# Performance work log

Measured on AMD Instinct MI355X. Metric: run time of the kernel, lower is better.

The kernel has to match this reference:

```python
import jax, jax.numpy as jnp
import numpy as np

NBINS = 256  # skimage threshold_otsu default
RGB_W = jnp.array([0.2989, 0.5870, 0.1140], dtype=jnp.float32)  # tf.image.rgb_to_grayscale weights


def threshold_otsu(img):
    """Global Otsu threshold over all pixels, matching skimage.filters.threshold_otsu."""
    vmin = img.min()
    vmax = img.max()
    edges = jnp.linspace(vmin, vmax, NBINS + 1)
    centers = (edges[:-1] + edges[1:]) * 0.5
    hist = jnp.histogram(img.ravel(), bins=edges)[0].astype(jnp.float32)
    # class probabilities / cumulative weights
    w1 = jnp.cumsum(hist)                      # weight of class <= t
    w2 = jnp.cumsum(hist[::-1])[::-1]          # weight of class > t
    hc = hist * centers
    s1 = jnp.cumsum(hc)
    s2 = jnp.cumsum(hc[::-1])[::-1]
    m1 = s1 / jnp.maximum(w1, 1.0)
    m2 = s2 / jnp.maximum(w2, 1.0)
    # inter-class variance at each split point
    var12 = w1[:-1] * w2[1:] * (m1[:-1] - m2[1:]) ** 2
    idx = jnp.argmax(var12)
    return centers[idx]


def setup_inputs() -> dict:
    key = jax.random.key(0)
    inputs = jax.random.uniform(key, (32, 128, 2048, 3), dtype=jnp.float32)
    return {"inputs": inputs}


def reference(inputs) -> jnp.ndarray:
    # rgb_to_grayscale on first 3 channels, keep channel dim -> [B,H,W,1]
    gray = jnp.einsum('bhwc,c->bhw', inputs[..., :3].astype(jnp.float32), RGB_W)[..., None]
    thresh = threshold_otsu(gray)
    binarized = (gray > thresh).astype(jnp.float32)   # [B,H,W,1]
    # channels == 3 -> tile grayscale binarization back to 3 channels
    binarized = jnp.tile(binarized, (1, 1, 1, 3))
    return binarized
```

## Files before the change

### kernel.cpp

```cpp
#include <hip/hip_runtime.h>

static constexpr int HIST_OFF   = 2;
static constexpr int EDGES_OFF  = 258;
static constexpr int VMIN_OFF   = 515;
static constexpr int DELTA_OFF  = 516;
static constexpr int INVD_OFF   = 517;
static constexpr int THRESH_OFF = 518;
static constexpr size_t GRAY_BYTE_OFF = 4096;

typedef float nfloat4 __attribute__((ext_vector_type(4)));

__device__ __forceinline__ unsigned fkey(float x) {
    unsigned u = __float_as_uint(x);
    return (u & 0x80000000u) ? ~u : (u | 0x80000000u);
}
__device__ __forceinline__ float keyf(unsigned k) {
    return (k & 0x80000000u) ? __uint_as_float(k & 0x7FFFFFFFu)
                             : __uint_as_float(~k);
}

__device__ __forceinline__ float gray1(float r, float g, float b) {
    float t0 = __fmul_rn(r, 0.2989f);
    float t1 = __fmul_rn(g, 0.5870f);
    float t2 = __fmul_rn(b, 0.1140f);
    return __fadd_rn(__fadd_rn(t0, t1), t2);
}

__device__ __forceinline__ float permf(int dst_addr, float v) {
    return __int_as_float(
        __builtin_amdgcn_ds_permute(dst_addr, __float_as_int(v)));
}
__device__ __forceinline__ float selk(float a, float b, float c, int k) {
    return (k == 0) ? a : ((k == 1) ? b : c);
}

__global__ void init_kernel(unsigned* __restrict__ wsu) {
    int i = threadIdx.x;
    if (i < 256) wsu[HIST_OFF + i] = 0u;
    if (i == 0) { wsu[0] = 0xFFFFFFFFu; wsu[1] = 0u; }
}

__global__ void __launch_bounds__(256)
gray_minmax_fast(const float* __restrict__ in, float* __restrict__ gray,
                 unsigned* __restrict__ wsu, int npix4) {
    __shared__ unsigned smn[4], smx[4];
    const nfloat4* in4 = (const nfloat4*)in;
    nfloat4* gray4 = (nfloat4*)gray;
    const int nf4 = npix4 * 3;
    const int lane = threadIdx.x & 63;
    const int gw = (blockIdx.x * blockDim.x + threadIdx.x) >> 6;
    unsigned mn = 0xFFFFFFFFu, mx = 0u;

    const int s3 = lane % 3;
    const int ka = (3 - s3) % 3;
    const int kb = (ka + 1) % 3;
    const int kc = (ka + 2) % 3;
    const int da = 4 * ((64 * ka + lane) / 3);
    const int db = 4 * ((64 * kb + lane) / 3);
    const int dc = 4 * ((64 * kc + lane) / 3);

    const int wbase4 = gw * 768;

    nfloat4 c[4][3];
    bool full[4];
#pragma unroll
    for (int r = 0; r < 4; ++r) {
        int rb = wbase4 + r * 192;
        full[r] = (rb + 192 <= nf4);
        if (full[r]) {
#pragma unroll
            for (int k = 0; k < 3; ++k)
                c[r][k] = __builtin_nontemporal_load(&in4[rb + 64 * k + lane]);
        }
    }
#pragma unroll
    for (int r = 0; r < 4; ++r) {
        const int gbase = gw * 256 + r * 64;
        nfloat4 d0, d1, d2;
        bool have = false;
        if (full[r]) {
            d0.x = permf(da, selk(c[r][0].x, c[r][1].x, c[r][2].x, ka));
            d0.y = permf(da, selk(c[r][0].y, c[r][1].y, c[r][2].y, ka));
            d0.z = permf(da, selk(c[r][0].z, c[r][1].z, c[r][2].z, ka));
            d0.w = permf(da, selk(c[r][0].w, c[r][1].w, c[r][2].w, ka));
            d1.x = permf(db, selk(c[r][0].x, c[r][1].x, c[r][2].x, kb));
            d1.y = permf(db, selk(c[r][0].y, c[r][1].y, c[r][2].y, kb));
            d1.z = permf(db, selk(c[r][0].z, c[r][1].z, c[r][2].z, kb));
            d1.w = permf(db, selk(c[r][0].w, c[r][1].w, c[r][2].w, kb));
            d2.x = permf(dc, selk(c[r][0].x, c[r][1].x, c[r][2].x, kc));
            d2.y = permf(dc, selk(c[r][0].y, c[r][1].y, c[r][2].y, kc));
            d2.z = permf(dc, selk(c[r][0].z, c[r][1].z, c[r][2].z, kc));
            d2.w = permf(dc, selk(c[r][0].w, c[r][1].w, c[r][2].w, kc));
            have = true;
        } else {
            int g = gbase + lane;
            if (g < npix4) {
                const nfloat4* p = in4 + (size_t)g * 3;
                d0 = p[0]; d1 = p[1]; d2 = p[2];
                have = true;
            }
        }
        if (have) {
            float g0 = gray1(d0.x, d0.y, d0.z);
            float g1 = gray1(d0.w, d1.x, d1.y);
            float g2 = gray1(d1.z, d1.w, d2.x);
            float g3 = gray1(d2.y, d2.z, d2.w);
            gray4[gbase + lane] = (nfloat4){g0, g1, g2, g3};
            unsigned k0 = fkey(g0), k1 = fkey(g1), k2 = fkey(g2), k3 = fkey(g3);
            mn = min(mn, min(min(k0, k1), min(k2, k3)));
            mx = max(mx, max(max(k0, k1), max(k2, k3)));
        }
    }
    for (int off = 32; off > 0; off >>= 1) {
        mn = min(mn, (unsigned)__shfl_xor((int)mn, off, 64));
        mx = max(mx, (unsigned)__shfl_xor((int)mx, off, 64));
    }
    int wave = threadIdx.x >> 6;
    if ((threadIdx.x & 63) == 0) { smn[wave] = mn; smx[wave] = mx; }
    __syncthreads();
    if (threadIdx.x == 0) {
        mn = min(min(smn[0], smn[1]), min(smn[2], smn[3]));
        mx = max(max(smx[0], smx[1]), max(smx[2], smx[3]));
        atomicMin(&wsu[0], mn);
        atomicMax(&wsu[1], mx);
    }
}

__global__ void __launch_bounds__(256)
gray_minmax_generic(const float* __restrict__ in, float* __restrict__ gray,
                    unsigned* __restrict__ wsu, int npix4) {
    __shared__ unsigned smn[4], smx[4];
    const float4* in4 = (const float4*)in;
    const int stride = gridDim.x * blockDim.x;
    unsigned mn = 0xFFFFFFFFu, mx = 0u;
    for (int t = blockIdx.x * blockDim.x + threadIdx.x; t < npix4; t += stride) {
        const float4* p = in4 + (size_t)t * 3;
        float4 c0 = p[0], c1 = p[1], c2 = p[2];
        float g0 = gray1(c0.x, c0.y, c0.z);
        float g1 = gray1(c0.w, c1.x, c1.y);
        float g2 = gray1(c1.z, c1.w, c2.x);
        float g3 = gray1(c2.y, c2.z, c2.w);
        if (gray) ((float4*)gray)[t] = make_float4(g0, g1, g2, g3);
        unsigned k0 = fkey(g0), k1 = fkey(g1), k2 = fkey(g2), k3 = fkey(g3);
        mn = min(mn, min(min(k0, k1), min(k2, k3)));
        mx = max(mx, max(max(k0, k1), max(k2, k3)));
    }
    for (int off = 32; off > 0; off >>= 1) {
        mn = min(mn, (unsigned)__shfl_xor((int)mn, off, 64));
        mx = max(mx, (unsigned)__shfl_xor((int)mx, off, 64));
    }
    int wave = threadIdx.x >> 6;
    if ((threadIdx.x & 63) == 0) { smn[wave] = mn; smx[wave] = mx; }
    __syncthreads();
    if (threadIdx.x == 0) {
        mn = min(min(smn[0], smn[1]), min(smn[2], smn[3]));
        mx = max(max(smx[0], smx[1]), max(smx[2], smx[3]));
        atomicMin(&wsu[0], mn);
        atomicMax(&wsu[1], mx);
    }
}

__global__ void edges_kernel(const unsigned* __restrict__ wsu,
                             float* __restrict__ wsf) {
    float vmin = keyf(wsu[0]);
    float vmax = keyf(wsu[1]);
    float delta = __fdiv_rn(__fsub_rn(vmax, vmin), 256.0f);
    int i = threadIdx.x;
    if (i <= 256) {
        float e = (i == 256) ? vmax
                             : __fadd_rn(vmin, __fmul_rn((float)i, delta));
        wsf[EDGES_OFF + i] = e;
    }
    if (i == 0) {
        wsf[VMIN_OFF]  = vmin;
        wsf[DELTA_OFF] = delta;
        wsf[INVD_OFF]  = (delta > 0.0f) ? __fdiv_rn(1.0f, delta) : 0.0f;
    }
}

__device__ __forceinline__ void bin4(float x0, float x1, float x2, float x3,
                                     const float* eds, float vmin, float invd,
                                     unsigned* lh) {
    float xs[4] = {x0, x1, x2, x3};
#pragma unroll
    for (int j = 0; j < 4; ++j) {
        float x = xs[j];
        int b = (int)(__fmul_rn(__fsub_rn(x, vmin), invd));
        b = b < 0 ? 0 : (b > 255 ? 255 : b);
        while (b < 255 && x >= eds[b + 1]) ++b;
        while (b > 0 && x < eds[b]) --b;
        atomicAdd(&lh[b], 1u);
    }
}

__global__ void __launch_bounds__(256)
hist_kernel(const float* __restrict__ gray, const float* __restrict__ in,
            const float* __restrict__ wsf, unsigned* __restrict__ wsu,
            int npix4) {
    __shared__ float eds[257];
    __shared__ unsigned lh[256];
    for (int i = threadIdx.x; i < 257; i += blockDim.x)
        eds[i] = wsf[EDGES_OFF + i];
    if (threadIdx.x < 256) lh[threadIdx.x] = 0u;
    __syncthreads();
    const float vmin = eds[0];
    const float invd = wsf[INVD_OFF];
    const int stride = gridDim.x * blockDim.x;
    const int base = blockIdx.x * blockDim.x + threadIdx.x;

    if (gray && base + 7 * stride < npix4) {
        float4 g[8];
#pragma unroll
        for (int j = 0; j < 8; ++j) g[j] = ((const float4*)gray)[base + j * stride];
#pragma unroll
        for (int j = 0; j < 8; ++j)
            bin4(g[j].x, g[j].y, g[j].z, g[j].w, eds, vmin, invd, lh);
    } else {
        for (int t = base; t < npix4; t += stride) {
            float4 g4;
            if (gray) g4 = ((const float4*)gray)[t];
            else {
                const float4* p = (const float4*)in + (size_t)t * 3;
                float4 c0 = p[0], c1 = p[1], c2 = p[2];
                g4 = make_float4(gray1(c0.x, c0.y, c0.z),
                                 gray1(c0.w, c1.x, c1.y),
                                 gray1(c1.z, c1.w, c2.x),
                                 gray1(c2.y, c2.z, c2.w));
            }
            bin4(g4.x, g4.y, g4.z, g4.w, eds, vmin, invd, lh);
        }
    }
    __syncthreads();
    if (threadIdx.x < 256 && lh[threadIdx.x] != 0u)
        atomicAdd(&wsu[HIST_OFF + threadIdx.x], lh[threadIdx.x]);
}

__global__ void otsu_kernel(const unsigned* __restrict__ wsu,
                            float* __restrict__ wsf) {
    __shared__ float histf[256];
    __shared__ float centers[256];
    __shared__ float w2a[256];
    __shared__ float s2a[256];
    int i = threadIdx.x;
    float e0 = wsf[EDGES_OFF + i];
    float e1 = wsf[EDGES_OFF + i + 1];
    centers[i] = __fmul_rn(__fadd_rn(e0, e1), 0.5f);
    histf[i] = (float)wsu[HIST_OFF + i];
    __syncthreads();
    if (i == 0) {
        float w = 0.0f, s = 0.0f;
        for (int t = 255; t >= 0; --t) {
            w = __fadd_rn(w, histf[t]);
            s = __fadd_rn(s, __fmul_rn(histf[t], centers[t]));
            w2a[t] = w;
            s2a[t] = s;
        }
        float w1 = 0.0f, s1 = 0.0f, best = -1.0f;
        int bidx = 0;
        for (int t = 0; t < 255; ++t) {
            w1 = __fadd_rn(w1, histf[t]);
            s1 = __fadd_rn(s1, __fmul_rn(histf[t], centers[t]));
            float m1 = __fdiv_rn(s1, fmaxf(w1, 1.0f));
            float m2 = __fdiv_rn(s2a[t + 1], fmaxf(w2a[t + 1], 1.0f));
            float d  = __fsub_rn(m1, m2);
            float v  = __fmul_rn(__fmul_rn(w1, w2a[t + 1]), __fmul_rn(d, d));
            if (v > best) { best = v; bidx = t; }
        }
        wsf[THRESH_OFF] = centers[bidx];
    }
}

__global__ void __launch_bounds__(256)
binarize_fast(const float* __restrict__ gray, const float* __restrict__ wsf,
              float* __restrict__ out, int npix4) {
    const float thr = wsf[THRESH_OFF];
    const nfloat4* gray4 = (const nfloat4*)gray;
    nfloat4* out4 = (nfloat4*)out;
    const int lane = threadIdx.x & 63;
    const int gw = (blockIdx.x * blockDim.x + threadIdx.x) >> 6;

    const int ma = lane / 3,         qa = lane % 3;
    const int mb = (64 + lane) / 3,  qb = (64 + lane) % 3;
    const int mc = (128 + lane) / 3, qc = (128 + lane) % 3;

    nfloat4 g[4];
    bool full[4];
#pragma unroll
    for (int r = 0; r < 4; ++r) {
        int gbase = gw * 256 + r * 64;
        full[r] = (gbase + 64 <= npix4);
        if (full[r]) g[r] = gray4[gbase + lane];
    }
#pragma unroll
    for (int r = 0; r < 4; ++r) {
        const int gbase = gw * 256 + r * 64;
        if (full[r]) {
            unsigned u = (g[r].x > thr ? 1u : 0u) |
                         (g[r].y > thr ? 0x100u : 0u) |
                         (g[r].z > thr ? 0x10000u : 0u) |
                         (g[r].w > thr ? 0x1000000u : 0u);
            const int rb = 3 * gbase;
#pragma unroll
            for (int k = 0; k < 3; ++k) {
                int m = (k == 0) ? ma : (k == 1) ? mb : mc;
                int q = (k == 0) ? qa : (k == 1) ? qb : qc;
                unsigned w = (unsigned)__builtin_amdgcn_ds_bpermute(4 * m,
                                                                    (int)u);
                float h0 = (w & 0xffu)        ? 1.0f : 0.0f;
                float h1 = (w & 0xff00u)      ? 1.0f : 0.0f;
                float h2 = (w & 0xff0000u)    ? 1.0f : 0.0f;
                float h3 = (w & 0xff000000u)  ? 1.0f : 0.0f;
                nfloat4 o;
                o.x = (q == 0) ? h0 : (q == 1) ? h1 : h2;
                o.y = (q == 0) ? h0 : (q == 1) ? h1 : h3;
                o.z = (q == 0) ? h0 : (q == 1) ? h2 : h3;
                o.w = (q == 0) ? h1 : (q == 1) ? h2 : h3;
                __builtin_nontemporal_store(o, &out4[rb + 64 * k + lane]);
            }
        } else {
            int t = gbase + lane;
            if (t < npix4) {
                nfloat4 gg = gray4[t];
                float b0 = (gg.x > thr) ? 1.0f : 0.0f;
                float b1 = (gg.y > thr) ? 1.0f : 0.0f;
                float b2 = (gg.z > thr) ? 1.0f : 0.0f;
                float b3 = (gg.w > thr) ? 1.0f : 0.0f;
                nfloat4* o = out4 + (size_t)t * 3;
                __builtin_nontemporal_store((nfloat4){b0, b0, b0, b1}, &o[0]);
                __builtin_nontemporal_store((nfloat4){b1, b1, b2, b2}, &o[1]);
                __builtin_nontemporal_store((nfloat4){b2, b3, b3, b3}, &o[2]);
            }
        }
    }
}

__global__ void __launch_bounds__(256)
binarize_generic(const float* __restrict__ gray, const float* __restrict__ in,
                 const float* __restrict__ wsf, float* __restrict__ out,
                 int npix4) {
    const float thr = wsf[THRESH_OFF];
    const int stride = gridDim.x * blockDim.x;
    nfloat4* out4 = (nfloat4*)out;
    for (int t = blockIdx.x * blockDim.x + threadIdx.x; t < npix4; t += stride) {
        float4 g4;
        if (gray) g4 = ((const float4*)gray)[t];
        else {
            const float4* p = (const float4*)in + (size_t)t * 3;
            float4 c0 = p[0], c1 = p[1], c2 = p[2];
            g4 = make_float4(gray1(c0.x, c0.y, c0.z),
                             gray1(c0.w, c1.x, c1.y),
                             gray1(c1.z, c1.w, c2.x),
                             gray1(c2.y, c2.z, c2.w));
        }
        float b0 = (g4.x > thr) ? 1.0f : 0.0f;
        float b1 = (g4.y > thr) ? 1.0f : 0.0f;
        float b2 = (g4.z > thr) ? 1.0f : 0.0f;
        float b3 = (g4.w > thr) ? 1.0f : 0.0f;
        nfloat4* o = out4 + (size_t)t * 3;
        o[0] = (nfloat4){b0, b0, b0, b1};
        o[1] = (nfloat4){b1, b1, b2, b2};
        o[2] = (nfloat4){b2, b3, b3, b3};
    }
}

extern "C" void kernel_launch(void* const* d_in, const int* in_sizes, int n_in,
                              void* d_out, int out_size, void* d_ws,
                              size_t ws_size, hipStream_t stream) {
    const float* in = (const float*)d_in[0];
    float* out = (float*)d_out;
    int npix  = out_size / 3;
    int npix4 = npix / 4;
    unsigned* wsu = (unsigned*)d_ws;
    float* wsf = (float*)d_ws;
    size_t need = GRAY_BYTE_OFF + (size_t)npix * sizeof(float);
    float* gray = (ws_size >= need)
                      ? (float*)((char*)d_ws + GRAY_BYTE_OFF)
                      : nullptr;

    hipLaunchKernelGGL(init_kernel, dim3(1), dim3(256), 0, stream, wsu);
    int fblocks = (npix4 + 1023) / 1024;
    if (gray) {
        hipLaunchKernelGGL(gray_minmax_fast, dim3(fblocks), dim3(256), 0,
                           stream, in, gray, wsu, npix4);
    } else {
        hipLaunchKernelGGL(gray_minmax_generic, dim3(2048), dim3(256), 0,
                           stream, in, gray, wsu, npix4);
    }
    hipLaunchKernelGGL(edges_kernel, dim3(1), dim3(320), 0, stream, wsu, wsf);
    hipLaunchKernelGGL(hist_kernel, dim3(1024), dim3(256), 0, stream,
                       gray, in, wsf, wsu, npix4);
    hipLaunchKernelGGL(otsu_kernel, dim3(1), dim3(256), 0, stream, wsu, wsf);
    if (gray) {
        hipLaunchKernelGGL(binarize_fast, dim3(fblocks), dim3(256), 0, stream,
                           gray, wsf, out, npix4);
    } else {
        hipLaunchKernelGGL(binarize_generic, dim3(2048), dim3(256), 0, stream,
                           gray, in, wsf, out, npix4);
    }
}
```

Baseline: 287.2 us.

## Fuse gray/minmax, histogram, Otsu and binarize into one cooperative persistent kernel

Replaces the multi-kernel pipeline with a single cooperative kernel. Each wave holds its grayscale values in registers across two grid-wide syncs, so the gray buffer is never written to or re-read from global memory. The Otsu threshold is computed redundantly per block. The input loads are software-pipelined with double buffering. The cost is two grid syncs, a fixed 1024-block grid whose tiles must cover all pixels, and a redundant serial Otsu scan in every block.

```diff
diff --git a/kernel.cpp b/kernel.cpp
--- a/kernel.cpp
+++ b/kernel.cpp
@@ -1,4 +1,7 @@
 #include <hip/hip_runtime.h>
+#include <hip/hip_cooperative_groups.h>
+
+namespace cg = cooperative_groups;
 
 static constexpr int HIST_OFF   = 2;
 static constexpr int EDGES_OFF  = 258;
@@ -18,20 +21,21 @@
     return (k & 0x80000000u) ? __uint_as_float(k & 0x7FFFFFFFu)
                              : __uint_as_float(~k);
 }
-
 __device__ __forceinline__ float gray1(float r, float g, float b) {
     float t0 = __fmul_rn(r, 0.2989f);
     float t1 = __fmul_rn(g, 0.5870f);
     float t2 = __fmul_rn(b, 0.1140f);
     return __fadd_rn(__fadd_rn(t0, t1), t2);
 }
-
 __device__ __forceinline__ float permf(int dst_addr, float v) {
     return __int_as_float(
         __builtin_amdgcn_ds_permute(dst_addr, __float_as_int(v)));
 }
 __device__ __forceinline__ float selk(float a, float b, float c, int k) {
     return (k == 0) ? a : ((k == 1) ? b : c);
+}
+__device__ __forceinline__ unsigned aload(const unsigned* p) {
+    return __hip_atomic_load(p, __ATOMIC_RELAXED, __HIP_MEMORY_SCOPE_AGENT);
 }
 
 __global__ void init_kernel(unsigned* __restrict__ wsu) {
@@ -40,57 +44,67 @@
     if (i == 0) { wsu[0] = 0xFFFFFFFFu; wsu[1] = 0u; }
 }
 
-__global__ void __launch_bounds__(256)
-gray_minmax_fast(const float* __restrict__ in, float* __restrict__ gray,
-                 unsigned* __restrict__ wsu, int npix4) {
-    __shared__ unsigned smn[4], smx[4];
+__global__ void __launch_bounds__(256, 4)
+fused_kernel(const float* __restrict__ in, float* __restrict__ out,
+             unsigned* __restrict__ wsu, int npix4) {
+    cg::grid_group grid = cg::this_grid();
+    __shared__ float eds[257];
+    __shared__ unsigned lh[256];
+    __shared__ float histf[256], centers[256], w2a[256], s2a[256];
+    __shared__ unsigned smn[4], smx[4], skey[2];
+    __shared__ float sthr;
+
     const nfloat4* in4 = (const nfloat4*)in;
-    nfloat4* gray4 = (nfloat4*)gray;
-    const int nf4 = npix4 * 3;
+    nfloat4* out4 = (nfloat4*)out;
     const int lane = threadIdx.x & 63;
     const int gw = (blockIdx.x * blockDim.x + threadIdx.x) >> 6;
-    unsigned mn = 0xFFFFFFFFu, mx = 0u;
+    const int gtile = gw * 512;
+    const int wbase4 = gw * 1536;
 
     const int s3 = lane % 3;
-    const int ka = (3 - s3) % 3;
-    const int kb = (ka + 1) % 3;
-    const int kc = (ka + 2) % 3;
+    const int ka = (3 - s3) % 3, kb = (ka + 1) % 3, kc = (ka + 2) % 3;
     const int da = 4 * ((64 * ka + lane) / 3);
     const int db = 4 * ((64 * kb + lane) / 3);
     const int dc = 4 * ((64 * kc + lane) / 3);
-
-    const int wbase4 = gw * 768;
-
-    nfloat4 c[4][3];
-    bool full[4];
-#pragma unroll
-    for (int r = 0; r < 4; ++r) {
-        int rb = wbase4 + r * 192;
-        full[r] = (rb + 192 <= nf4);
-        if (full[r]) {
+    const int ma = lane / 3,         qa = lane % 3;
+    const int mb = (64 + lane) / 3,  qb = (64 + lane) % 3;
+    const int mc = (128 + lane) / 3, qc = (128 + lane) % 3;
+
+    bool full[8];
+#pragma unroll
+    for (int r = 0; r < 8; ++r) full[r] = (gtile + r * 64 + 64 <= npix4);
+
+    float gr[8][4];
+    unsigned mn = 0xFFFFFFFFu, mx = 0u;
+    nfloat4 cb[2][3];
+    if (full[0]) {
+#pragma unroll
+        for (int k = 0; k < 3; ++k) cb[0][k] = in4[wbase4 + 64 * k + lane];
+    }
+#pragma unroll
+    for (int r = 0; r < 8; ++r) {
+        const int cur = r & 1, nxt = cur ^ 1;
+        if (r + 1 < 8 && full[r + 1]) {
 #pragma unroll
             for (int k = 0; k < 3; ++k)
-                c[r][k] = __builtin_nontemporal_load(&in4[rb + 64 * k + lane]);
-        }
-    }
-#pragma unroll
-    for (int r = 0; r < 4; ++r) {
-        const int gbase = gw * 256 + r * 64;
+                cb[nxt][k] = in4[wbase4 + (r + 1) * 192 + 64 * k + lane];
+        }
+        const int gbase = gtile + r * 64;
         nfloat4 d0, d1, d2;
         bool have = false;
         if (full[r]) {
-            d0.x = permf(da, selk(c[r][0].x, c[r][1].x, c[r][2].x, ka));
-            d0.y = permf(da, selk(c[r][0].y, c[r][1].y, c[r][2].y, ka));
-            d0.z = permf(da, selk(c[r][0].z, c[r][1].z, c[r][2].z, ka));
-            d0.w = permf(da, selk(c[r][0].w, c[r][1].w, c[r][2].w, ka));
-            d1.x = permf(db, selk(c[r][0].x, c[r][1].x, c[r][2].x, kb));
-            d1.y = permf(db, selk(c[r][0].y, c[r][1].y, c[r][2].y, kb));
-            d1.z = permf(db, selk(c[r][0].z, c[r][1].z, c[r][2].z, kb));
-            d1.w = permf(db, selk(c[r][0].w, c[r][1].w, c[r][2].w, kb));
-            d2.x = permf(dc, selk(c[r][0].x, c[r][1].x, c[r][2].x, kc));
-            d2.y = permf(dc, selk(c[r][0].y, c[r][1].y, c[r][2].y, kc));
-            d2.z = permf(dc, selk(c[r][0].z, c[r][1].z, c[r][2].z, kc));
-            d2.w = permf(dc, selk(c[r][0].w, c[r][1].w, c[r][2].w, kc));
+            d0.x = permf(da, selk(cb[cur][0].x, cb[cur][1].x, cb[cur][2].x, ka));
+            d0.y = permf(da, selk(cb[cur][0].y, cb[cur][1].y, cb[cur][2].y, ka));
+            d0.z = permf(da, selk(cb[cur][0].z, cb[cur][1].z, cb[cur][2].z, ka));
+            d0.w = permf(da, selk(cb[cur][0].w, cb[cur][1].w, cb[cur][2].w, ka));
+            d1.x = permf(db, selk(cb[cur][0].x, cb[cur][1].x, cb[cur][2].x, kb));
+            d1.y = permf(db, selk(cb[cur][0].y, cb[cur][1].y, cb[cur][2].y, kb));
+            d1.z = permf(db, selk(cb[cur][0].z, cb[cur][1].z, cb[cur][2].z, kb));
+            d1.w = permf(db, selk(cb[cur][0].w, cb[cur][1].w, cb[cur][2].w, kb));
+            d2.x = permf(dc, selk(cb[cur][0].x, cb[cur][1].x, cb[cur][2].x, kc));
+            d2.y = permf(dc, selk(cb[cur][0].y, cb[cur][1].y, cb[cur][2].y, kc));
+            d2.z = permf(dc, selk(cb[cur][0].z, cb[cur][1].z, cb[cur][2].z, kc));
+            d2.w = permf(dc, selk(cb[cur][0].w, cb[cur][1].w, cb[cur][2].w, kc));
             have = true;
         } else {
             int g = gbase + lane;
@@ -101,28 +115,137 @@
             }
         }
         if (have) {
-            float g0 = gray1(d0.x, d0.y, d0.z);
-            float g1 = gray1(d0.w, d1.x, d1.y);
-            float g2 = gray1(d1.z, d1.w, d2.x);
-            float g3 = gray1(d2.y, d2.z, d2.w);
-            gray4[gbase + lane] = (nfloat4){g0, g1, g2, g3};
-            unsigned k0 = fkey(g0), k1 = fkey(g1), k2 = fkey(g2), k3 = fkey(g3);
+            gr[r][0] = gray1(d0.x, d0.y, d0.z);
+            gr[r][1] = gray1(d0.w, d1.x, d1.y);
+            gr[r][2] = gray1(d1.z, d1.w, d2.x);
+            gr[r][3] = gray1(d2.y, d2.z, d2.w);
+            unsigned k0 = fkey(gr[r][0]), k1 = fkey(gr[r][1]);
+            unsigned k2 = fkey(gr[r][2]), k3 = fkey(gr[r][3]);
             mn = min(mn, min(min(k0, k1), min(k2, k3)));
             mx = max(mx, max(max(k0, k1), max(k2, k3)));
+        } else {
+            gr[r][0] = gr[r][1] = gr[r][2] = gr[r][3] = 0.0f;
         }
     }
     for (int off = 32; off > 0; off >>= 1) {
         mn = min(mn, (unsigned)__shfl_xor((int)mn, off, 64));
         mx = max(mx, (unsigned)__shfl_xor((int)mx, off, 64));
     }
-    int wave = threadIdx.x >> 6;
-    if ((threadIdx.x & 63) == 0) { smn[wave] = mn; smx[wave] = mx; }
+    {
+        int wave = threadIdx.x >> 6;
+        if ((threadIdx.x & 63) == 0) { smn[wave] = mn; smx[wave] = mx; }
+        __syncthreads();
+        if (threadIdx.x == 0) {
+            unsigned bmn = min(min(smn[0], smn[1]), min(smn[2], smn[3]));
+            unsigned bmx = max(max(smx[0], smx[1]), max(smx[2], smx[3]));
+            atomicMin(&wsu[0], bmn);
+            atomicMax(&wsu[1], bmx);
+        }
+    }
+    grid.sync();
+
+    if (threadIdx.x == 0) { skey[0] = aload(&wsu[0]); skey[1] = aload(&wsu[1]); }
+    __syncthreads();
+    const float vmin = keyf(skey[0]);
+    const float vmax = keyf(skey[1]);
+    const float delta = __fdiv_rn(__fsub_rn(vmax, vmin), 256.0f);
+    const float invd = (delta > 0.0f) ? __fdiv_rn(1.0f, delta) : 0.0f;
+    if (threadIdx.x < 256)
+        eds[threadIdx.x] =
+            __fadd_rn(vmin, __fmul_rn((float)threadIdx.x, delta));
+    if (threadIdx.x == 0) eds[256] = vmax;
+    if (threadIdx.x < 256) lh[threadIdx.x] = 0u;
+    __syncthreads();
+
+#pragma unroll
+    for (int r = 0; r < 8; ++r) {
+        const int g = gtile + r * 64 + lane;
+        if (full[r] || g < npix4) {
+#pragma unroll
+            for (int j = 0; j < 4; ++j) {
+                float x = gr[r][j];
+                int b = (int)(__fmul_rn(__fsub_rn(x, vmin), invd));
+                b = b < 0 ? 0 : (b > 255 ? 255 : b);
+                while (b < 255 && x >= eds[b + 1]) ++b;
+                while (b > 0 && x < eds[b]) --b;
+                atomicAdd(&lh[b], 1u);
+            }
+        }
+    }
+    __syncthreads();
+    if (threadIdx.x < 256 && lh[threadIdx.x] != 0u)
+        atomicAdd(&wsu[HIST_OFF + threadIdx.x], lh[threadIdx.x]);
+    grid.sync();
+
+    if (threadIdx.x < 256) {
+        float e0 = eds[threadIdx.x], e1 = eds[threadIdx.x + 1];
+        centers[threadIdx.x] = __fmul_rn(__fadd_rn(e0, e1), 0.5f);
+        histf[threadIdx.x] = (float)aload(&wsu[HIST_OFF + threadIdx.x]);
+    }
     __syncthreads();
     if (threadIdx.x == 0) {
-        mn = min(min(smn[0], smn[1]), min(smn[2], smn[3]));
-        mx = max(max(smx[0], smx[1]), max(smx[2], smx[3]));
-        atomicMin(&wsu[0], mn);
-        atomicMax(&wsu[1], mx);
+        float w = 0.0f, s = 0.0f;
+        for (int t = 255; t >= 0; --t) {
+            w = __fadd_rn(w, histf[t]);
+            s = __fadd_rn(s, __fmul_rn(histf[t], centers[t]));
+            w2a[t] = w;
+            s2a[t] = s;
+        }
+        float w1 = 0.0f, s1 = 0.0f, best = -1.0f;
+        int bidx = 0;
+        for (int t = 0; t < 255; ++t) {
+            w1 = __fadd_rn(w1, histf[t]);
+            s1 = __fadd_rn(s1, __fmul_rn(histf[t], centers[t]));
+            float m1 = __fdiv_rn(s1, fmaxf(w1, 1.0f));
+            float m2 = __fdiv_rn(s2a[t + 1], fmaxf(w2a[t + 1], 1.0f));
+            float d  = __fsub_rn(m1, m2);
+            float v  = __fmul_rn(__fmul_rn(w1, w2a[t + 1]), __fmul_rn(d, d));
+            if (v > best) { best = v; bidx = t; }
+        }
+        sthr = centers[bidx];
+    }
+    __syncthreads();
+    const float thr = sthr;
+
+#pragma unroll
+    for (int r = 0; r < 8; ++r) {
+        const int gbase = gtile + r * 64;
+        if (full[r]) {
+            unsigned u = (gr[r][0] > thr ? 1u : 0u) |
+                         (gr[r][1] > thr ? 0x100u : 0u) |
+                         (gr[r][2] > thr ? 0x10000u : 0u) |
+                         (gr[r][3] > thr ? 0x1000000u : 0u);
+            const int rb = 3 * gbase;
+#pragma unroll
+            for (int k = 0; k < 3; ++k) {
+                int m = (k == 0) ? ma : (k == 1) ? mb : mc;
+                int q = (k == 0) ? qa : (k == 1) ? qb : qc;
+                unsigned w = (unsigned)__builtin_amdgcn_ds_bpermute(4 * m,
+                                                                    (int)u);
+                float h0 = (w & 0xffu)       ? 1.0f : 0.0f;
+                float h1 = (w & 0xff00u)     ? 1.0f : 0.0f;
+                float h2 = (w & 0xff0000u)   ? 1.0f : 0.0f;
+                float h3 = (w & 0xff000000u) ? 1.0f : 0.0f;
+                nfloat4 o;
+                o.x = (q == 0) ? h0 : (q == 1) ? h1 : h2;
+                o.y = (q == 0) ? h0 : (q == 1) ? h1 : h3;
+                o.z = (q == 0) ? h0 : (q == 1) ? h2 : h3;
+                o.w = (q == 0) ? h1 : (q == 1) ? h2 : h3;
+                __builtin_nontemporal_store(o, &out4[rb + 64 * k + lane]);
+            }
+        } else {
+            int t = gbase + lane;
+            if (t < npix4) {
+                float b0 = (gr[r][0] > thr) ? 1.0f : 0.0f;
+                float b1 = (gr[r][1] > thr) ? 1.0f : 0.0f;
+                float b2 = (gr[r][2] > thr) ? 1.0f : 0.0f;
+                float b3 = (gr[r][3] > thr) ? 1.0f : 0.0f;
+                nfloat4* o = out4 + (size_t)t * 3;
+                __builtin_nontemporal_store((nfloat4){b0, b0, b0, b1}, &o[0]);
+                __builtin_nontemporal_store((nfloat4){b1, b1, b2, b2}, &o[1]);
+                __builtin_nontemporal_store((nfloat4){b2, b3, b3, b3}, &o[2]);
+            }
+        }
     }
 }
 
@@ -206,29 +329,16 @@
     const float vmin = eds[0];
     const float invd = wsf[INVD_OFF];
     const int stride = gridDim.x * blockDim.x;
-    const int base = blockIdx.x * blockDim.x + threadIdx.x;
-
-    if (gray && base + 7 * stride < npix4) {
-        float4 g[8];
-#pragma unroll
-        for (int j = 0; j < 8; ++j) g[j] = ((const float4*)gray)[base + j * stride];
-#pragma unroll
-        for (int j = 0; j < 8; ++j)
-            bin4(g[j].x, g[j].y, g[j].z, g[j].w, eds, vmin, invd, lh);
-    } else {
-        for (int t = base; t < npix4; t += stride) {
-            float4 g4;
-            if (gray) g4 = ((const float4*)gray)[t];
-            else {
-                const float4* p = (const float4*)in + (size_t)t * 3;
-                float4 c0 = p[0], c1 = p[1], c2 = p[2];
-                g4 = make_float4(gray1(c0.x, c0.y, c0.z),
-                                 gray1(c0.w, c1.x, c1.y),
-                                 gray1(c1.z, c1.w, c2.x),
-                                 gray1(c2.y, c2.z, c2.w));
-            }
-            bin4(g4.x, g4.y, g4.z, g4.w, eds, vmin, invd, lh);
-        }
+    for (int t = blockIdx.x * blockDim.x + threadIdx.x; t < npix4; t += stride) {
+        float4 g4;
+        if (gray) g4 = ((const float4*)gray)[t];
+        else {
+            const float4* p = (const float4*)in + (size_t)t * 3;
+            float4 c0 = p[0], c1 = p[1], c2 = p[2];
+            g4 = make_float4(gray1(c0.x, c0.y, c0.z), gray1(c0.w, c1.x, c1.y),
+                             gray1(c1.z, c1.w, c2.x), gray1(c2.y, c2.z, c2.w));
+        }
+        bin4(g4.x, g4.y, g4.z, g4.w, eds, vmin, invd, lh);
     }
     __syncthreads();
     if (threadIdx.x < 256 && lh[threadIdx.x] != 0u)
@@ -267,70 +377,6 @@
             if (v > best) { best = v; bidx = t; }
         }
         wsf[THRESH_OFF] = centers[bidx];
-    }
-}
-
-__global__ void __launch_bounds__(256)
-binarize_fast(const float* __restrict__ gray, const float* __restrict__ wsf,
-              float* __restrict__ out, int npix4) {
-    const float thr = wsf[THRESH_OFF];
-    const nfloat4* gray4 = (const nfloat4*)gray;
-    nfloat4* out4 = (nfloat4*)out;
-    const int lane = threadIdx.x & 63;
-    const int gw = (blockIdx.x * blockDim.x + threadIdx.x) >> 6;
-
-    const int ma = lane / 3,         qa = lane % 3;
-    const int mb = (64 + lane) / 3,  qb = (64 + lane) % 3;
-    const int mc = (128 + lane) / 3, qc = (128 + lane) % 3;
-
-    nfloat4 g[4];
-    bool full[4];
-#pragma unroll
-    for (int r = 0; r < 4; ++r) {
-        int gbase = gw * 256 + r * 64;
-        full[r] = (gbase + 64 <= npix4);
-        if (full[r]) g[r] = gray4[gbase + lane];
-    }
-#pragma unroll
-    for (int r = 0; r < 4; ++r) {
-        const int gbase = gw * 256 + r * 64;
-        if (full[r]) {
-            unsigned u = (g[r].x > thr ? 1u : 0u) |
-                         (g[r].y > thr ? 0x100u : 0u) |
-                         (g[r].z > thr ? 0x10000u : 0u) |
-                         (g[r].w > thr ? 0x1000000u : 0u);
-            const int rb = 3 * gbase;
-#pragma unroll
-            for (int k = 0; k < 3; ++k) {
-                int m = (k == 0) ? ma : (k == 1) ? mb : mc;
-                int q = (k == 0) ? qa : (k == 1) ? qb : qc;
-                unsigned w = (unsigned)__builtin_amdgcn_ds_bpermute(4 * m,
-                                                                    (int)u);
-                float h0 = (w & 0xffu)        ? 1.0f : 0.0f;
-                float h1 = (w & 0xff00u)      ? 1.0f : 0.0f;
-                float h2 = (w & 0xff0000u)    ? 1.0f : 0.0f;
-                float h3 = (w & 0xff000000u)  ? 1.0f : 0.0f;
-                nfloat4 o;
-                o.x = (q == 0) ? h0 : (q == 1) ? h1 : h2;
-                o.y = (q == 0) ? h0 : (q == 1) ? h1 : h3;
-                o.z = (q == 0) ? h0 : (q == 1) ? h2 : h3;
-                o.w = (q == 0) ? h1 : (q == 1) ? h2 : h3;
-                __builtin_nontemporal_store(o, &out4[rb + 64 * k + lane]);
-            }
-        } else {
-            int t = gbase + lane;
-            if (t < npix4) {
-                nfloat4 gg = gray4[t];
-                float b0 = (gg.x > thr) ? 1.0f : 0.0f;
-                float b1 = (gg.y > thr) ? 1.0f : 0.0f;
-                float b2 = (gg.z > thr) ? 1.0f : 0.0f;
-                float b3 = (gg.w > thr) ? 1.0f : 0.0f;
-                nfloat4* o = out4 + (size_t)t * 3;
-                __builtin_nontemporal_store((nfloat4){b0, b0, b0, b1}, &o[0]);
-                __builtin_nontemporal_store((nfloat4){b1, b1, b2, b2}, &o[1]);
-                __builtin_nontemporal_store((nfloat4){b2, b3, b3, b3}, &o[2]);
-            }
-        }
     }
 }
 
@@ -347,10 +393,8 @@
         else {
             const float4* p = (const float4*)in + (size_t)t * 3;
             float4 c0 = p[0], c1 = p[1], c2 = p[2];
-            g4 = make_float4(gray1(c0.x, c0.y, c0.z),
-                             gray1(c0.w, c1.x, c1.y),
-                             gray1(c1.z, c1.w, c2.x),
-                             gray1(c2.y, c2.z, c2.w));
+            g4 = make_float4(gray1(c0.x, c0.y, c0.z), gray1(c0.w, c1.x, c1.y),
+                             gray1(c1.z, c1.w, c2.x), gray1(c2.y, c2.z, c2.w));
         }
         float b0 = (g4.x > thr) ? 1.0f : 0.0f;
         float b1 = (g4.y > thr) ? 1.0f : 0.0f;
@@ -372,29 +416,24 @@
     int npix4 = npix / 4;
     unsigned* wsu = (unsigned*)d_ws;
     float* wsf = (float*)d_ws;
+
+    hipLaunchKernelGGL(init_kernel, dim3(1), dim3(256), 0, stream, wsu);
+
+    void* args[] = {(void*)&in, (void*)&out, (void*)&wsu, (void*)&npix4};
+    hipError_t err = hipLaunchCooperativeKernel(
+        (const void*)fused_kernel, dim3(1024), dim3(256), args, 0, stream);
+    if (err == hipSuccess) return;
+
     size_t need = GRAY_BYTE_OFF + (size_t)npix * sizeof(float);
     float* gray = (ws_size >= need)
                       ? (float*)((char*)d_ws + GRAY_BYTE_OFF)
                       : nullptr;
-
-    hipLaunchKernelGGL(init_kernel, dim3(1), dim3(256), 0, stream, wsu);
-    int fblocks = (npix4 + 1023) / 1024;
-    if (gray) {
-        hipLaunchKernelGGL(gray_minmax_fast, dim3(fblocks), dim3(256), 0,
-                           stream, in, gray, wsu, npix4);
-    } else {
-        hipLaunchKernelGGL(gray_minmax_generic, dim3(2048), dim3(256), 0,
-                           stream, in, gray, wsu, npix4);
-    }
+    hipLaunchKernelGGL(gray_minmax_generic, dim3(2048), dim3(256), 0, stream,
+                       in, gray, wsu, npix4);
     hipLaunchKernelGGL(edges_kernel, dim3(1), dim3(320), 0, stream, wsu, wsf);
     hipLaunchKernelGGL(hist_kernel, dim3(1024), dim3(256), 0, stream,
                        gray, in, wsf, wsu, npix4);
     hipLaunchKernelGGL(otsu_kernel, dim3(1), dim3(256), 0, stream, wsu, wsf);
-    if (gray) {
-        hipLaunchKernelGGL(binarize_fast, dim3(fblocks), dim3(256), 0, stream,
-                           gray, wsf, out, npix4);
-    } else {
-        hipLaunchKernelGGL(binarize_generic, dim3(2048), dim3(256), 0, stream,
-                           gray, in, wsf, out, npix4);
-    }
-}
+    hipLaunchKernelGGL(binarize_generic, dim3(2048), dim3(256), 0, stream,
+                       gray, in, wsf, out, npix4);
+}
```

New measurement: 457.0 us. 59.1% more time.

## Stage gray/minmax input through LDS with async global-to-LDS double-buffered loads

Applied to the files above, without the earlier changes.

The grayscale-plus-minmax kernel no longer deinterleaves RGB in registers with ds_permute shuffles. It now loads each wave's chunk directly into LDS with global_load_lds and double-buffers across four sub-tiles, using manual s_waitcnt on vmcnt. Each lane then reads its three float4s from LDS, which removes the permute/select work and overlaps the next load with compute. The trade-offs are the hand-coded waitcnt encodings, which are fragile, the loss of nontemporal loads, and a fast path that now requires npix4 divisible by 1024.

```diff
diff --git a/kernel.cpp b/kernel.cpp
--- a/kernel.cpp
+++ b/kernel.cpp
@@ -10,6 +10,11 @@
 
 typedef float nfloat4 __attribute__((ext_vector_type(4)));
 
+#define GLOAD_LDS16(gp, lp)                                                    \
+    __builtin_amdgcn_global_load_lds(                                          \
+        (const __attribute__((address_space(1))) void*)(gp),                   \
+        (__attribute__((address_space(3))) void*)(lp), 16, 0, 0)
+
 __device__ __forceinline__ unsigned fkey(float x) {
     unsigned u = __float_as_uint(x);
     return (u & 0x80000000u) ? ~u : (u | 0x80000000u);
@@ -18,7 +23,6 @@
     return (k & 0x80000000u) ? __uint_as_float(k & 0x7FFFFFFFu)
                              : __uint_as_float(~k);
 }
-
 __device__ __forceinline__ float gray1(float r, float g, float b) {
     float t0 = __fmul_rn(r, 0.2989f);
     float t1 = __fmul_rn(g, 0.5870f);
@@ -26,14 +30,6 @@
     return __fadd_rn(__fadd_rn(t0, t1), t2);
 }
 
-__device__ __forceinline__ float permf(int dst_addr, float v) {
-    return __int_as_float(
-        __builtin_amdgcn_ds_permute(dst_addr, __float_as_int(v)));
-}
-__device__ __forceinline__ float selk(float a, float b, float c, int k) {
-    return (k == 0) ? a : ((k == 1) ? b : c);
-}
-
 __global__ void init_kernel(unsigned* __restrict__ wsu) {
     int i = threadIdx.x;
     if (i < 256) wsu[HIST_OFF + i] = 0u;
@@ -41,82 +37,51 @@
 }
 
 __global__ void __launch_bounds__(256)
-gray_minmax_fast(const float* __restrict__ in, float* __restrict__ gray,
-                 unsigned* __restrict__ wsu, int npix4) {
+gray_minmax_async(const float* __restrict__ in, float* __restrict__ gray,
+                  unsigned* __restrict__ wsu, int npix4) {
+    __shared__ float4 sbuf[4][2][192];
     __shared__ unsigned smn[4], smx[4];
-    const nfloat4* in4 = (const nfloat4*)in;
-    nfloat4* gray4 = (nfloat4*)gray;
-    const int nf4 = npix4 * 3;
+    const float4* in4 = (const float4*)in;
+    float4* gray4 = (float4*)gray;
     const int lane = threadIdx.x & 63;
-    const int gw = (blockIdx.x * blockDim.x + threadIdx.x) >> 6;
+    const int w = threadIdx.x >> 6;
+    const int gw = blockIdx.x * 4 + w;
+    const size_t wbase4 = (size_t)gw * 768;
     unsigned mn = 0xFFFFFFFFu, mx = 0u;
 
-    const int s3 = lane % 3;
-    const int ka = (3 - s3) % 3;
-    const int kb = (ka + 1) % 3;
-    const int kc = (ka + 2) % 3;
-    const int da = 4 * ((64 * ka + lane) / 3);
-    const int db = 4 * ((64 * kb + lane) / 3);
-    const int dc = 4 * ((64 * kc + lane) / 3);
-
-    const int wbase4 = gw * 768;
-
-    nfloat4 c[4][3];
-    bool full[4];
-#pragma unroll
-    for (int r = 0; r < 4; ++r) {
-        int rb = wbase4 + r * 192;
-        full[r] = (rb + 192 <= nf4);
-        if (full[r]) {
+#pragma unroll
+    for (int k = 0; k < 3; ++k)
+        GLOAD_LDS16(in4 + wbase4 + 64 * k + lane, &sbuf[w][0][64 * k]);
+
+#pragma unroll
+    for (int t = 0; t < 4; ++t) {
+        const int cb = t & 1;
+        if (t < 3) {
 #pragma unroll
             for (int k = 0; k < 3; ++k)
-                c[r][k] = __builtin_nontemporal_load(&in4[rb + 64 * k + lane]);
-        }
-    }
-#pragma unroll
-    for (int r = 0; r < 4; ++r) {
-        const int gbase = gw * 256 + r * 64;
-        nfloat4 d0, d1, d2;
-        bool have = false;
-        if (full[r]) {
-            d0.x = permf(da, selk(c[r][0].x, c[r][1].x, c[r][2].x, ka));
-            d0.y = permf(da, selk(c[r][0].y, c[r][1].y, c[r][2].y, ka));
-            d0.z = permf(da, selk(c[r][0].z, c[r][1].z, c[r][2].z, ka));
-            d0.w = permf(da, selk(c[r][0].w, c[r][1].w, c[r][2].w, ka));
-            d1.x = permf(db, selk(c[r][0].x, c[r][1].x, c[r][2].x, kb));
-            d1.y = permf(db, selk(c[r][0].y, c[r][1].y, c[r][2].y, kb));
-            d1.z = permf(db, selk(c[r][0].z, c[r][1].z, c[r][2].z, kb));
-            d1.w = permf(db, selk(c[r][0].w, c[r][1].w, c[r][2].w, kb));
-            d2.x = permf(dc, selk(c[r][0].x, c[r][1].x, c[r][2].x, kc));
-            d2.y = permf(dc, selk(c[r][0].y, c[r][1].y, c[r][2].y, kc));
-            d2.z = permf(dc, selk(c[r][0].z, c[r][1].z, c[r][2].z, kc));
-            d2.w = permf(dc, selk(c[r][0].w, c[r][1].w, c[r][2].w, kc));
-            have = true;
+                GLOAD_LDS16(in4 + wbase4 + (size_t)(t + 1) * 192 + 64 * k + lane,
+                            &sbuf[w][cb ^ 1][64 * k]);
+            __builtin_amdgcn_s_waitcnt(0x0F73);
         } else {
-            int g = gbase + lane;
-            if (g < npix4) {
-                const nfloat4* p = in4 + (size_t)g * 3;
-                d0 = p[0]; d1 = p[1]; d2 = p[2];
-                have = true;
-            }
-        }
-        if (have) {
-            float g0 = gray1(d0.x, d0.y, d0.z);
-            float g1 = gray1(d0.w, d1.x, d1.y);
-            float g2 = gray1(d1.z, d1.w, d2.x);
-            float g3 = gray1(d2.y, d2.z, d2.w);
-            gray4[gbase + lane] = (nfloat4){g0, g1, g2, g3};
-            unsigned k0 = fkey(g0), k1 = fkey(g1), k2 = fkey(g2), k3 = fkey(g3);
-            mn = min(mn, min(min(k0, k1), min(k2, k3)));
-            mx = max(mx, max(max(k0, k1), max(k2, k3)));
-        }
+            __builtin_amdgcn_s_waitcnt(0x0F71);
+        }
+        float4 c0 = sbuf[w][cb][3 * lane + 0];
+        float4 c1 = sbuf[w][cb][3 * lane + 1];
+        float4 c2 = sbuf[w][cb][3 * lane + 2];
+        float g0 = gray1(c0.x, c0.y, c0.z);
+        float g1 = gray1(c0.w, c1.x, c1.y);
+        float g2 = gray1(c1.z, c1.w, c2.x);
+        float g3 = gray1(c2.y, c2.z, c2.w);
+        gray4[(size_t)gw * 256 + t * 64 + lane] = make_float4(g0, g1, g2, g3);
+        unsigned k0 = fkey(g0), k1 = fkey(g1), k2 = fkey(g2), k3 = fkey(g3);
+        mn = min(mn, min(min(k0, k1), min(k2, k3)));
+        mx = max(mx, max(max(k0, k1), max(k2, k3)));
     }
     for (int off = 32; off > 0; off >>= 1) {
         mn = min(mn, (unsigned)__shfl_xor((int)mn, off, 64));
         mx = max(mx, (unsigned)__shfl_xor((int)mx, off, 64));
     }
-    int wave = threadIdx.x >> 6;
-    if ((threadIdx.x & 63) == 0) { smn[wave] = mn; smx[wave] = mx; }
+    if (lane == 0) { smn[w] = mn; smx[w] = mx; }
     __syncthreads();
     if (threadIdx.x == 0) {
         mn = min(min(smn[0], smn[1]), min(smn[2], smn[3]));
@@ -207,7 +172,6 @@
     const float invd = wsf[INVD_OFF];
     const int stride = gridDim.x * blockDim.x;
     const int base = blockIdx.x * blockDim.x + threadIdx.x;
-
     if (gray && base + 7 * stride < npix4) {
         float4 g[8];
 #pragma unroll
@@ -222,10 +186,8 @@
             else {
                 const float4* p = (const float4*)in + (size_t)t * 3;
                 float4 c0 = p[0], c1 = p[1], c2 = p[2];
-                g4 = make_float4(gray1(c0.x, c0.y, c0.z),
-                                 gray1(c0.w, c1.x, c1.y),
-                                 gray1(c1.z, c1.w, c2.x),
-                                 gray1(c2.y, c2.z, c2.w));
+                g4 = make_float4(gray1(c0.x, c0.y, c0.z), gray1(c0.w, c1.x, c1.y),
+                                 gray1(c1.z, c1.w, c2.x), gray1(c2.y, c2.z, c2.w));
             }
             bin4(g4.x, g4.y, g4.z, g4.w, eds, vmin, invd, lh);
         }
@@ -278,7 +240,6 @@
     nfloat4* out4 = (nfloat4*)out;
     const int lane = threadIdx.x & 63;
     const int gw = (blockIdx.x * blockDim.x + threadIdx.x) >> 6;
-
     const int ma = lane / 3,         qa = lane % 3;
     const int mb = (64 + lane) / 3,  qb = (64 + lane) % 3;
     const int mc = (128 + lane) / 3, qc = (128 + lane) % 3;
@@ -306,10 +267,10 @@
                 int q = (k == 0) ? qa : (k == 1) ? qb : qc;
                 unsigned w = (unsigned)__builtin_amdgcn_ds_bpermute(4 * m,
                                                                     (int)u);
-                float h0 = (w & 0xffu)        ? 1.0f : 0.0f;
-                float h1 = (w & 0xff00u)      ? 1.0f : 0.0f;
-                float h2 = (w & 0xff0000u)    ? 1.0f : 0.0f;
-                float h3 = (w & 0xff000000u)  ? 1.0f : 0.0f;
+                float h0 = (w & 0xffu)       ? 1.0f : 0.0f;
+                float h1 = (w & 0xff00u)     ? 1.0f : 0.0f;
+                float h2 = (w & 0xff0000u)   ? 1.0f : 0.0f;
+                float h3 = (w & 0xff000000u) ? 1.0f : 0.0f;
                 nfloat4 o;
                 o.x = (q == 0) ? h0 : (q == 1) ? h1 : h2;
                 o.y = (q == 0) ? h0 : (q == 1) ? h1 : h3;
@@ -347,10 +308,8 @@
         else {
             const float4* p = (const float4*)in + (size_t)t * 3;
             float4 c0 = p[0], c1 = p[1], c2 = p[2];
-            g4 = make_float4(gray1(c0.x, c0.y, c0.z),
-                             gray1(c0.w, c1.x, c1.y),
-                             gray1(c1.z, c1.w, c2.x),
-                             gray1(c2.y, c2.z, c2.w));
+            g4 = make_float4(gray1(c0.x, c0.y, c0.z), gray1(c0.w, c1.x, c1.y),
+                             gray1(c1.z, c1.w, c2.x), gray1(c2.y, c2.z, c2.w));
         }
         float b0 = (g4.x > thr) ? 1.0f : 0.0f;
         float b1 = (g4.y > thr) ? 1.0f : 0.0f;
@@ -378,9 +337,8 @@
                       : nullptr;
 
     hipLaunchKernelGGL(init_kernel, dim3(1), dim3(256), 0, stream, wsu);
-    int fblocks = (npix4 + 1023) / 1024;
-    if (gray) {
-        hipLaunchKernelGGL(gray_minmax_fast, dim3(fblocks), dim3(256), 0,
+    if (gray && npix4 % 1024 == 0) {
+        hipLaunchKernelGGL(gray_minmax_async, dim3(npix4 / 1024), dim3(256), 0,
                            stream, in, gray, wsu, npix4);
     } else {
         hipLaunchKernelGGL(gray_minmax_generic, dim3(2048), dim3(256), 0,
@@ -391,8 +349,8 @@
                        gray, in, wsf, wsu, npix4);
     hipLaunchKernelGGL(otsu_kernel, dim3(1), dim3(256), 0, stream, wsu, wsf);
     if (gray) {
-        hipLaunchKernelGGL(binarize_fast, dim3(fblocks), dim3(256), 0, stream,
-                           gray, wsf, out, npix4);
+        hipLaunchKernelGGL(binarize_fast, dim3((npix4 + 1023) / 1024),
+                           dim3(256), 0, stream, gray, wsf, out, npix4);
     } else {
         hipLaunchKernelGGL(binarize_generic, dim3(2048), dim3(256), 0, stream,
                            gray, in, wsf, out, npix4);
```

Result: no change. 282.2 us (-1.8%).
